# Performance work log

Hardware: AMD Instinct MI355X
Metric: run time of the kernel (lower is better)

## Reference

```python
import jax, jax.numpy as jnp
import numpy as np
from jax import lax

EPS = 1e-8
DN = ('NCHW', 'OIHW', 'NCHW')


def setup_inputs() -> dict:
    key = jax.random.key(0)
    k1, k2 = jax.random.split(key)
    inputs = jax.random.normal(k1, (16, 3, 512, 512), dtype=jnp.float32)
    template = jax.random.normal(k2, (16, 3, 21, 21), dtype=jnp.float32)
    return {"inputs": inputs, "template": template}


def _normalize_template(template):
    # Z-normalize each (batch, channel) plane independently, then divide by
    # patch element count (matches NCC.__init__).
    B, C, th, tw = template.shape
    t = template.reshape(B, C, th * tw)
    t = t - jnp.mean(t, axis=-1, keepdims=True)
    t = t / (jnp.std(t, axis=-1, keepdims=True) + EPS)  # ddof=0 == unbiased=False
    return t.reshape(B, C, th, tw) / (th * tw)


def reference(inputs, template):
    B, C, H, W = inputs.shape
    th, tw = template.shape[2], template.shape[3]
    nt = _normalize_template(template)

    # Per-(b,c) depthwise cross-correlation (the grouped conv with eye-masked
    # weights is exactly a depthwise conv with per-sample filters).
    x = inputs.reshape(1, B * C, H, W)
    w = nt.reshape(B * C, 1, th, tw)
    res = lax.conv_general_dilated(x, w, (1, 1), 'VALID',
                                   dimension_numbers=DN,
                                   feature_group_count=B * C)
    res = res.reshape(B, C, res.shape[2], res.shape[3])  # (B,C,Hout,Wout)

    # Local (patch) std per channel via box filter (shared across batch).
    box = jnp.full((C, 1, th, tw), 1.0 / (th * tw), dtype=inputs.dtype)
    mean = lax.conv_general_dilated(inputs, box, (1, 1), 'VALID',
                                    dimension_numbers=DN, feature_group_count=C)
    mean_sq = lax.conv_general_dilated(inputs * inputs, box, (1, 1), 'VALID',
                                       dimension_numbers=DN, feature_group_count=C)
    std = jnp.sqrt(mean_sq - mean * mean + EPS)

    return res / (std + EPS)
```

## Files before the change

### kernel.cpp

```cpp
#include <hip/hip_runtime.h>
#include <math.h>

typedef __attribute__((ext_vector_type(8)))  short short8;
typedef __attribute__((ext_vector_type(16))) float f32x16;

#define NPLANE 48
#define H 512
#define W 512
#define TH 21
#define OH 492
#define OW 492
#define EPSF 1e-8f

#define STRIDE 168
#define SEG_ROWS 84

#define BONES_HOFF (4128768u / 2)

__device__ inline unsigned short f2bf(float f) {
    unsigned u = __float_as_uint(f);
    return (unsigned short)((u + 0x7FFFu + ((u >> 16) & 1u)) >> 16);
}
__device__ inline float bf2f(unsigned s) {
    return __uint_as_float(s << 16);
}
__device__ inline unsigned cvtpk(float lo, float hi) {
    unsigned r;
    asm("v_cvt_pk_bf16_f32 %0, %1, %2" : "=v"(r) : "v"(lo), "v"(hi));
    return r;
}

__global__ void build_b_kernel(const float* __restrict__ tpl,
                               unsigned short* __restrict__ ws16) {
    __shared__ float sm[2];
    const int plane = blockIdx.x;
    const float* t = tpl + plane * 441;
    const int tid = threadIdx.x;
    if (tid < 64) {
        float s = 0.f, s2 = 0.f;
        for (int k = tid; k < 441; k += 64) {
            float x = t[k];
            s += x; s2 += x * x;
        }
#pragma unroll
        for (int o = 32; o >= 1; o >>= 1) {
            s  += __shfl_down(s, o);
            s2 += __shfl_down(s2, o);
        }
        if (tid == 0) {
            float mean = s / 441.f;
            float var = fmaxf(s2 / 441.f - mean * mean, 0.f);
            sm[0] = mean;
            sm[1] = 1.f / ((sqrtf(var) + EPSF) * 441.f);
        }
    }
    __syncthreads();
    const float mean = sm[0], scale = sm[1];

    unsigned short* bc = ws16 + (size_t)plane * 43008;
    for (int i = tid; i < 43008; i += 256) {
        int j = i & 7, lane = (i >> 3) & 63, s = (i >> 9) & 3, u = i >> 11;
        int k = ((lane >> 5) << 3) + j, n = lane & 31;
        int v = 16 * s + k - n;
        float val = (v >= 0 && v < TH) ? (t[u * 21 + v] - mean) * scale : 0.f;
        bc[i] = f2bf(val);
    }
    if (plane == 0) {
        unsigned short* bo = ws16 + BONES_HOFF;
        const unsigned short one = f2bf(1.f);
        for (int i = tid; i < 2048; i += 256) {
            int j = i & 7, lane = (i >> 3) & 63, s = (i >> 9) & 3;
            int k = ((lane >> 5) << 3) + j, n = lane & 31;
            int v = 16 * s + k - n;
            bo[i] = (v >= 0 && v < TH) ? one : (unsigned short)0;
        }
    }
}

__global__ __launch_bounds__(512, 6) void ncc_fused_kernel(
    const float* __restrict__ in, const unsigned short* __restrict__ ws16,
    float* __restrict__ out) {
    __shared__ short seg[SEG_ROWS * STRIDE];
    __shared__ short vbuf[64 * STRIDE];

    const int plane = blockIdx.z;
    const int x0 = blockIdx.x * 128;
    const int y0 = blockIdx.y * 64;
    const int tid = threadIdx.x;
    const int lane = tid & 63;
    const int wid = tid >> 6;
    const int tr = wid & 1;
    const int tc = wid >> 1;
    const float* src = in + (size_t)plane * H * W;

    for (int i = tid; i < SEG_ROWS * 20; i += 512) {
        int row = i / 20, s8 = i - row * 20;
        int gy = y0 + row, gx = x0 + s8 * 8;
        if (gy < H && gx + 7 < W) {
            float4 a = *(const float4*)(src + gy * W + gx);
            float4 b = *(const float4*)(src + gy * W + gx + 4);
            uint4 v;
            v.x = cvtpk(a.x, a.y);
            v.y = cvtpk(a.z, a.w);
            v.z = cvtpk(b.x, b.y);
            v.w = cvtpk(b.z, b.w);
            *(uint4*)&seg[row * STRIDE + s8 * 8] = v;
        } else {
            short8 val;
#pragma unroll
            for (int e = 0; e < 8; ++e) {
                float xv = (gy < H && gx + e < W) ? src[gy * W + gx + e] : 0.f;
                val[e] = (short)f2bf(xv);
            }
            *(short8*)&seg[row * STRIDE + s8 * 8] = val;
        }
    }
    __syncthreads();

    const int m = lane & 31;
    const int half = lane >> 5;
    const int abase = (tr * 32 + m) * STRIDE + tc * 32 + half * 8;
    const unsigned short* bc = ws16 + (size_t)plane * 43008 + lane * 8;

    f32x16 acc;
#pragma unroll
    for (int e = 0; e < 16; ++e) acc[e] = 0.f;

    auto corr_step = [&](int u, short8* bf) {
        short8 af[4];
#pragma unroll
        for (int s = 0; s < 4; ++s)
            af[s] = *(const short8*)&seg[abase + u * STRIDE + s * 16];
#pragma unroll
        for (int s = 0; s < 4; ++s)
            acc = __builtin_amdgcn_mfma_f32_32x32x16_bf16(af[s], bf[s], acc,
                                                          0, 0, 0);
    };

    short8 bA[4], bB[4];
#pragma unroll
    for (int s = 0; s < 4; ++s)
        bA[s] = *(const short8*)(bc + s * 512);

    for (int u = 0; u < TH - 1; u += 2) {
#pragma unroll
        for (int s = 0; s < 4; ++s)
            bB[s] = *(const short8*)(bc + ((u + 1) * 4 + s) * 512);
        corr_step(u, bA);
#pragma unroll
        for (int s = 0; s < 4; ++s)
            bA[s] = *(const short8*)(bc + ((u + 2) * 4 + s) * 512);
        corr_step(u + 1, bB);
    }
    corr_step(TH - 1, bA);

    const unsigned short* bo16 = ws16 + BONES_HOFF + lane * 8;
    short8 bones[4];
#pragma unroll
    for (int s = 0; s < 4; ++s)
        bones[s] = *(const short8*)(bo16 + s * 512);

    auto vpass = [&](bool sq) {
        if (tid < 320) {
            const int q = tid / 80;
            const int c2 = (tid - q * 80) * 2;
            const int base = q * 16;
            float s0 = 0.f, s1 = 0.f;
#pragma unroll
            for (int r = 0; r < 20; ++r) {
                unsigned p = *(const unsigned*)&seg[(base + r) * STRIDE + c2];
                float a = bf2f(p & 0xffffu), b = bf2f(p >> 16);
                if (sq) { s0 = fmaf(a, a, s0); s1 = fmaf(b, b, s1); }
                else    { s0 += a; s1 += b; }
            }
#pragma unroll
            for (int yb = 0; yb < 16; yb += 8) {
                unsigned pin[8], pout[8];
#pragma unroll
                for (int r = 0; r < 8; ++r) {
                    pin[r]  = *(const unsigned*)
                        &seg[(base + yb + r + 20) * STRIDE + c2];
                    pout[r] = *(const unsigned*)
                        &seg[(base + yb + r) * STRIDE + c2];
                }
#pragma unroll
                for (int r = 0; r < 8; ++r) {
                    float a = bf2f(pin[r] & 0xffffu), b = bf2f(pin[r] >> 16);
                    if (sq) { s0 = fmaf(a, a, s0); s1 = fmaf(b, b, s1); }
                    else    { s0 += a; s1 += b; }
                    *(unsigned*)&vbuf[(base + yb + r) * STRIDE + c2] =
                        cvtpk(s0, s1);
                    float c = bf2f(pout[r] & 0xffffu), d = bf2f(pout[r] >> 16);
                    if (sq) { s0 = fmaf(-c, c, s0); s1 = fmaf(-d, d, s1); }
                    else    { s0 -= c; s1 -= d; }
                }
            }
        }
    };

    vpass(false);
    __syncthreads();

    f32x16 aS;
#pragma unroll
    for (int e = 0; e < 16; ++e) aS[e] = 0.f;
#pragma unroll
    for (int s = 0; s < 4; ++s) {
        short8 vf = *(const short8*)&vbuf[abase + s * 16];
        aS = __builtin_amdgcn_mfma_f32_32x32x16_bf16(vf, bones[s], aS,
                                                     0, 0, 0);
    }
    __syncthreads();

    vpass(true);
    __syncthreads();

    f32x16 aQ;
#pragma unroll
    for (int e = 0; e < 16; ++e) aQ[e] = 0.f;
#pragma unroll
    for (int s = 0; s < 4; ++s) {
        short8 qf = *(const short8*)&vbuf[abase + s * 16];
        aQ = __builtin_amdgcn_mfma_f32_32x32x16_bf16(qf, bones[s], aQ,
                                                     0, 0, 0);
    }

    const float invn = 1.f / 441.f;
    float* outp = out + (size_t)plane * OH * OW;
    const int gx = x0 + tc * 32 + m;
    if (gx < OW) {
#pragma unroll
        for (int r = 0; r < 16; ++r) {
            int gy = y0 + tr * 32 + (r & 3) + ((r >> 2) << 3) + half * 4;
            if (gy < OH) {
                float mean = aS[r] * invn;
                float msq = aQ[r] * invn;
                float var = fmaf(-mean, mean, msq) + EPSF;
                outp[(size_t)gy * OW + gx] =
                    acc[r] * __builtin_amdgcn_rsqf(var);
            }
        }
    }
}

extern "C" void kernel_launch(void* const* d_in, const int* in_sizes, int n_in,
                              void* d_out, int out_size, void* d_ws,
                              size_t ws_size, hipStream_t stream) {
    const float* inputs = (const float*)d_in[0];
    const float* tmpl = (const float*)d_in[1];
    float* out = (float*)d_out;
    unsigned short* ws16 = (unsigned short*)d_ws;

    build_b_kernel<<<NPLANE, 256, 0, stream>>>(tmpl, ws16);
    ncc_fused_kernel<<<dim3(4, 8, NPLANE), 512, 0, stream>>>(inputs, ws16, out);
}
```

Baseline: 167.2 us.

## Process two row tiles per block with register prefetch of next input segment

Each block now handles two vertically stacked 64-row output tiles instead of one, which halves the grid. While the first tile is being correlated, the input rows for the second tile are loaded into registers, then converted to bf16 and written into shared memory after the first tile's compute finishes. The goal is to hide global load latency behind MFMA work and to amortise the bones/B-fragment setup. In exchange it uses more registers, lowers the occupancy target from 6 to 4 blocks, and leaves fewer blocks to spread across the CUs.

```diff
diff --git a/kernel.cpp b/kernel.cpp
--- a/kernel.cpp
+++ b/kernel.cpp
@@ -77,7 +77,7 @@
     }
 }
 
-__global__ __launch_bounds__(512, 6) void ncc_fused_kernel(
+__global__ __launch_bounds__(512, 4) void ncc_fused_kernel(
     const float* __restrict__ in, const unsigned short* __restrict__ ws16,
     float* __restrict__ out) {
     __shared__ short seg[SEG_ROWS * STRIDE];
@@ -85,7 +85,7 @@
 
     const int plane = blockIdx.z;
     const int x0 = blockIdx.x * 128;
-    const int y0 = blockIdx.y * 64;
+    const int yb = blockIdx.y * 128;
     const int tid = threadIdx.x;
     const int lane = tid & 63;
     const int wid = tid >> 6;
@@ -95,7 +95,7 @@
 
     for (int i = tid; i < SEG_ROWS * 20; i += 512) {
         int row = i / 20, s8 = i - row * 20;
-        int gy = y0 + row, gx = x0 + s8 * 8;
+        int gy = yb + row, gx = x0 + s8 * 8;
         if (gy < H && gx + 7 < W) {
             float4 a = *(const float4*)(src + gy * W + gx);
             float4 b = *(const float4*)(src + gy * W + gx + 4);
@@ -115,50 +115,19 @@
             *(short8*)&seg[row * STRIDE + s8 * 8] = val;
         }
     }
-    __syncthreads();
 
     const int m = lane & 31;
     const int half = lane >> 5;
     const int abase = (tr * 32 + m) * STRIDE + tc * 32 + half * 8;
     const unsigned short* bc = ws16 + (size_t)plane * 43008 + lane * 8;
 
-    f32x16 acc;
-#pragma unroll
-    for (int e = 0; e < 16; ++e) acc[e] = 0.f;
-
-    auto corr_step = [&](int u, short8* bf) {
-        short8 af[4];
-#pragma unroll
-        for (int s = 0; s < 4; ++s)
-            af[s] = *(const short8*)&seg[abase + u * STRIDE + s * 16];
-#pragma unroll
-        for (int s = 0; s < 4; ++s)
-            acc = __builtin_amdgcn_mfma_f32_32x32x16_bf16(af[s], bf[s], acc,
-                                                          0, 0, 0);
-    };
-
-    short8 bA[4], bB[4];
-#pragma unroll
-    for (int s = 0; s < 4; ++s)
-        bA[s] = *(const short8*)(bc + s * 512);
-
-    for (int u = 0; u < TH - 1; u += 2) {
-#pragma unroll
-        for (int s = 0; s < 4; ++s)
-            bB[s] = *(const short8*)(bc + ((u + 1) * 4 + s) * 512);
-        corr_step(u, bA);
-#pragma unroll
-        for (int s = 0; s < 4; ++s)
-            bA[s] = *(const short8*)(bc + ((u + 2) * 4 + s) * 512);
-        corr_step(u + 1, bB);
-    }
-    corr_step(TH - 1, bA);
-
     const unsigned short* bo16 = ws16 + BONES_HOFF + lane * 8;
     short8 bones[4];
 #pragma unroll
     for (int s = 0; s < 4; ++s)
         bones[s] = *(const short8*)(bo16 + s * 512);
+
+    __syncthreads();
 
     auto vpass = [&](bool sq) {
         if (tid < 320) {
@@ -174,21 +143,21 @@
                 else    { s0 += a; s1 += b; }
             }
 #pragma unroll
-            for (int yb = 0; yb < 16; yb += 8) {
+            for (int yy = 0; yy < 16; yy += 8) {
                 unsigned pin[8], pout[8];
 #pragma unroll
                 for (int r = 0; r < 8; ++r) {
                     pin[r]  = *(const unsigned*)
-                        &seg[(base + yb + r + 20) * STRIDE + c2];
+                        &seg[(base + yy + r + 20) * STRIDE + c2];
                     pout[r] = *(const unsigned*)
-                        &seg[(base + yb + r) * STRIDE + c2];
+                        &seg[(base + yy + r) * STRIDE + c2];
                 }
 #pragma unroll
                 for (int r = 0; r < 8; ++r) {
                     float a = bf2f(pin[r] & 0xffffu), b = bf2f(pin[r] >> 16);
                     if (sq) { s0 = fmaf(a, a, s0); s1 = fmaf(b, b, s1); }
                     else    { s0 += a; s1 += b; }
-                    *(unsigned*)&vbuf[(base + yb + r) * STRIDE + c2] =
+                    *(unsigned*)&vbuf[(base + yy + r) * STRIDE + c2] =
                         cvtpk(s0, s1);
                     float c = bf2f(pout[r] & 0xffffu), d = bf2f(pout[r] >> 16);
                     if (sq) { s0 = fmaf(-c, c, s0); s1 = fmaf(-d, d, s1); }
@@ -198,48 +167,131 @@
         }
     };
 
-    vpass(false);
-    __syncthreads();
-
-    f32x16 aS;
-#pragma unroll
-    for (int e = 0; e < 16; ++e) aS[e] = 0.f;
-#pragma unroll
-    for (int s = 0; s < 4; ++s) {
-        short8 vf = *(const short8*)&vbuf[abase + s * 16];
-        aS = __builtin_amdgcn_mfma_f32_32x32x16_bf16(vf, bones[s], aS,
-                                                     0, 0, 0);
-    }
-    __syncthreads();
-
-    vpass(true);
-    __syncthreads();
-
-    f32x16 aQ;
-#pragma unroll
-    for (int e = 0; e < 16; ++e) aQ[e] = 0.f;
-#pragma unroll
-    for (int s = 0; s < 4; ++s) {
-        short8 qf = *(const short8*)&vbuf[abase + s * 16];
-        aQ = __builtin_amdgcn_mfma_f32_32x32x16_bf16(qf, bones[s], aQ,
-                                                     0, 0, 0);
-    }
-
-    const float invn = 1.f / 441.f;
-    float* outp = out + (size_t)plane * OH * OW;
-    const int gx = x0 + tc * 32 + m;
-    if (gx < OW) {
+    for (int ty = 0; ty < 2; ++ty) {
+        const int y0 = yb + ty * 64;
+
+        float4 ldA[4], ldB[4];
+        if (ty == 0) {
+#pragma unroll
+            for (int k = 0; k < 4; ++k) {
+                ldA[k] = make_float4(0.f, 0.f, 0.f, 0.f);
+                ldB[k] = make_float4(0.f, 0.f, 0.f, 0.f);
+                int i = tid + k * 512;
+                if (i < SEG_ROWS * 20) {
+                    int row = i / 20, s8 = i - row * 20;
+                    int gy = yb + 64 + row, gx = x0 + s8 * 8;
+                    if (gy < H && gx + 7 < W) {
+                        ldA[k] = *(const float4*)(src + gy * W + gx);
+                        ldB[k] = *(const float4*)(src + gy * W + gx + 4);
+                    } else {
+                        float t[8];
+#pragma unroll
+                        for (int e = 0; e < 8; ++e)
+                            t[e] = (gy < H && gx + e < W)
+                                       ? src[gy * W + gx + e] : 0.f;
+                        ldA[k] = make_float4(t[0], t[1], t[2], t[3]);
+                        ldB[k] = make_float4(t[4], t[5], t[6], t[7]);
+                    }
+                }
+            }
+        }
+
+        f32x16 acc;
+#pragma unroll
+        for (int e = 0; e < 16; ++e) acc[e] = 0.f;
+
+        auto corr_step = [&](int u, short8* bf) {
+            short8 af[4];
+#pragma unroll
+            for (int s = 0; s < 4; ++s)
+                af[s] = *(const short8*)&seg[abase + u * STRIDE + s * 16];
+#pragma unroll
+            for (int s = 0; s < 4; ++s)
+                acc = __builtin_amdgcn_mfma_f32_32x32x16_bf16(af[s], bf[s],
+                                                              acc, 0, 0, 0);
+        };
+
+        short8 bA[4], bB[4];
+#pragma unroll
+        for (int s = 0; s < 4; ++s)
+            bA[s] = *(const short8*)(bc + s * 512);
+
+        for (int u = 0; u < TH - 1; u += 2) {
+#pragma unroll
+            for (int s = 0; s < 4; ++s)
+                bB[s] = *(const short8*)(bc + ((u + 1) * 4 + s) * 512);
+            corr_step(u, bA);
+#pragma unroll
+            for (int s = 0; s < 4; ++s)
+                bA[s] = *(const short8*)(bc + ((u + 2) * 4 + s) * 512);
+            corr_step(u + 1, bB);
+        }
+        corr_step(TH - 1, bA);
+
+        vpass(false);
+        __syncthreads();
+
+        f32x16 aS;
+#pragma unroll
+        for (int e = 0; e < 16; ++e) aS[e] = 0.f;
+#pragma unroll
+        for (int s = 0; s < 4; ++s) {
+            short8 vf = *(const short8*)&vbuf[abase + s * 16];
+            aS = __builtin_amdgcn_mfma_f32_32x32x16_bf16(vf, bones[s], aS,
+                                                         0, 0, 0);
+        }
+        __syncthreads();
+
+        vpass(true);
+        __syncthreads();
+
+        f32x16 aQ;
+#pragma unroll
+        for (int e = 0; e < 16; ++e) aQ[e] = 0.f;
+#pragma unroll
+        for (int s = 0; s < 4; ++s) {
+            short8 qf = *(const short8*)&vbuf[abase + s * 16];
+            aQ = __builtin_amdgcn_mfma_f32_32x32x16_bf16(qf, bones[s], aQ,
+                                                         0, 0, 0);
+        }
+
+        if (ty == 0) {
+#pragma unroll
+            for (int k = 0; k < 4; ++k) {
+                int i = tid + k * 512;
+                if (i < SEG_ROWS * 20) {
+                    int row = i / 20, s8 = i - row * 20;
+                    uint4 v;
+                    v.x = cvtpk(ldA[k].x, ldA[k].y);
+                    v.y = cvtpk(ldA[k].z, ldA[k].w);
+                    v.z = cvtpk(ldB[k].x, ldB[k].y);
+                    v.w = cvtpk(ldB[k].z, ldB[k].w);
+                    *(uint4*)&seg[row * STRIDE + s8 * 8] = v;
+                }
+            }
+        }
+
+        const float invn = 1.f / 441.f;
+        float* outp = out + (size_t)plane * OH * OW;
+        float vout[16];
 #pragma unroll
         for (int r = 0; r < 16; ++r) {
-            int gy = y0 + tr * 32 + (r & 3) + ((r >> 2) << 3) + half * 4;
-            if (gy < OH) {
-                float mean = aS[r] * invn;
-                float msq = aQ[r] * invn;
-                float var = fmaf(-mean, mean, msq) + EPSF;
-                outp[(size_t)gy * OW + gx] =
-                    acc[r] * __builtin_amdgcn_rsqf(var);
-            }
-        }
+            float mean = aS[r] * invn;
+            float msq = aQ[r] * invn;
+            float var = fmaf(-mean, mean, msq) + EPSF;
+            vout[r] = acc[r] * __builtin_amdgcn_rsqf(var);
+        }
+        const int gx = x0 + tc * 32 + m;
+        if (gx < OW) {
+#pragma unroll
+            for (int r = 0; r < 16; ++r) {
+                int gy = y0 + tr * 32 + (r & 3) + ((r >> 2) << 3) + half * 4;
+                if (gy < OH)
+                    outp[(size_t)gy * OW + gx] = vout[r];
+            }
+        }
+
+        __syncthreads();
     }
 }
 
@@ -252,5 +304,5 @@
     unsigned short* ws16 = (unsigned short*)d_ws;
 
     build_b_kernel<<<NPLANE, 256, 0, stream>>>(tmpl, ws16);
-    ncc_fused_kernel<<<dim3(4, 8, NPLANE), 512, 0, stream>>>(inputs, ws16, out);
-}
+    ncc_fused_kernel<<<dim3(4, 4, NPLANE), 512, 0, stream>>>(inputs, ws16, out);
+}
```

New measurement: 583.8 us. 3.49x slower.

## Compute box-sum and box-square passes concurrently across all waves with separate buffers

Applied to the files above, without the earlier changes.

The sum and sum-of-squares vertical box passes move into separate LDS buffers and are spread over all 8 waves, 640 work units in total. The serial sequence of two vpass phases with four barriers becomes one phase with a single barrier. The ones-matrix B-fragment load is hoisted before the first barrier, and the two reduction MFMAs are interleaved. LDS use per block grows by one 64x168 buffer, and launch bounds drop from 6 to 4 blocks per CU, which may lower occupancy.

```diff
diff --git a/kernel.cpp b/kernel.cpp
--- a/kernel.cpp
+++ b/kernel.cpp
@@ -77,11 +77,12 @@
     }
 }
 
-__global__ __launch_bounds__(512, 6) void ncc_fused_kernel(
+__global__ __launch_bounds__(512, 4) void ncc_fused_kernel(
     const float* __restrict__ in, const unsigned short* __restrict__ ws16,
     float* __restrict__ out) {
     __shared__ short seg[SEG_ROWS * STRIDE];
-    __shared__ short vbuf[64 * STRIDE];
+    __shared__ short vsum[64 * STRIDE];
+    __shared__ short vsq[64 * STRIDE];
 
     const int plane = blockIdx.z;
     const int x0 = blockIdx.x * 128;
@@ -115,13 +116,20 @@
             *(short8*)&seg[row * STRIDE + s8 * 8] = val;
         }
     }
-    __syncthreads();
 
     const int m = lane & 31;
     const int half = lane >> 5;
     const int abase = (tr * 32 + m) * STRIDE + tc * 32 + half * 8;
     const unsigned short* bc = ws16 + (size_t)plane * 43008 + lane * 8;
 
+    const unsigned short* bo16 = ws16 + BONES_HOFF + lane * 8;
+    short8 bones[4];
+#pragma unroll
+    for (int s = 0; s < 4; ++s)
+        bones[s] = *(const short8*)(bo16 + s * 512);
+
+    __syncthreads();
+
     f32x16 acc;
 #pragma unroll
     for (int e = 0; e < 16; ++e) acc[e] = 0.f;
@@ -154,91 +162,80 @@
     }
     corr_step(TH - 1, bA);
 
-    const unsigned short* bo16 = ws16 + BONES_HOFF + lane * 8;
-    short8 bones[4];
-#pragma unroll
-    for (int s = 0; s < 4; ++s)
-        bones[s] = *(const short8*)(bo16 + s * 512);
-
-    auto vpass = [&](bool sq) {
-        if (tid < 320) {
-            const int q = tid / 80;
-            const int c2 = (tid - q * 80) * 2;
-            const int base = q * 16;
-            float s0 = 0.f, s1 = 0.f;
-#pragma unroll
-            for (int r = 0; r < 20; ++r) {
-                unsigned p = *(const unsigned*)&seg[(base + r) * STRIDE + c2];
-                float a = bf2f(p & 0xffffu), b = bf2f(p >> 16);
-                if (sq) { s0 = fmaf(a, a, s0); s1 = fmaf(b, b, s1); }
-                else    { s0 += a; s1 += b; }
+    auto unit = [&](int U) {
+        const int p = U / 320;
+        const int rem = U - p * 320;
+        const int q = rem / 80;
+        const int c2 = (rem - q * 80) * 2;
+        const int base = q * 16;
+        short* dst = p ? vsq : vsum;
+        float s0 = 0.f, s1 = 0.f;
+#pragma unroll
+        for (int r = 0; r < 20; ++r) {
+            unsigned pk = *(const unsigned*)&seg[(base + r) * STRIDE + c2];
+            float a = bf2f(pk & 0xffffu), b = bf2f(pk >> 16);
+            if (p) { s0 = fmaf(a, a, s0); s1 = fmaf(b, b, s1); }
+            else   { s0 += a; s1 += b; }
+        }
+#pragma unroll
+        for (int yy = 0; yy < 16; yy += 8) {
+            unsigned pin[8], pout[8];
+#pragma unroll
+            for (int r = 0; r < 8; ++r) {
+                pin[r]  = *(const unsigned*)
+                    &seg[(base + yy + r + 20) * STRIDE + c2];
+                pout[r] = *(const unsigned*)
+                    &seg[(base + yy + r) * STRIDE + c2];
             }
 #pragma unroll
-            for (int yb = 0; yb < 16; yb += 8) {
-                unsigned pin[8], pout[8];
-#pragma unroll
-                for (int r = 0; r < 8; ++r) {
-                    pin[r]  = *(const unsigned*)
-                        &seg[(base + yb + r + 20) * STRIDE + c2];
-                    pout[r] = *(const unsigned*)
-                        &seg[(base + yb + r) * STRIDE + c2];
-                }
-#pragma unroll
-                for (int r = 0; r < 8; ++r) {
-                    float a = bf2f(pin[r] & 0xffffu), b = bf2f(pin[r] >> 16);
-                    if (sq) { s0 = fmaf(a, a, s0); s1 = fmaf(b, b, s1); }
-                    else    { s0 += a; s1 += b; }
-                    *(unsigned*)&vbuf[(base + yb + r) * STRIDE + c2] =
-                        cvtpk(s0, s1);
-                    float c = bf2f(pout[r] & 0xffffu), d = bf2f(pout[r] >> 16);
-                    if (sq) { s0 = fmaf(-c, c, s0); s1 = fmaf(-d, d, s1); }
-                    else    { s0 -= c; s1 -= d; }
-                }
+            for (int r = 0; r < 8; ++r) {
+                float a = bf2f(pin[r] & 0xffffu), b = bf2f(pin[r] >> 16);
+                if (p) { s0 = fmaf(a, a, s0); s1 = fmaf(b, b, s1); }
+                else   { s0 += a; s1 += b; }
+                *(unsigned*)&dst[(base + yy + r) * STRIDE + c2] =
+                    cvtpk(s0, s1);
+                float c = bf2f(pout[r] & 0xffffu), d = bf2f(pout[r] >> 16);
+                if (p) { s0 = fmaf(-c, c, s0); s1 = fmaf(-d, d, s1); }
+                else   { s0 -= c; s1 -= d; }
             }
         }
     };
 
-    vpass(false);
+    unit(wid * 80 + lane);
+    if (lane < 16) unit(wid * 80 + 64 + lane);
+
     __syncthreads();
 
-    f32x16 aS;
-#pragma unroll
-    for (int e = 0; e < 16; ++e) aS[e] = 0.f;
+    f32x16 aS, aQ;
+#pragma unroll
+    for (int e = 0; e < 16; ++e) { aS[e] = 0.f; aQ[e] = 0.f; }
 #pragma unroll
     for (int s = 0; s < 4; ++s) {
-        short8 vf = *(const short8*)&vbuf[abase + s * 16];
+        short8 vf = *(const short8*)&vsum[abase + s * 16];
+        short8 qf = *(const short8*)&vsq[abase + s * 16];
         aS = __builtin_amdgcn_mfma_f32_32x32x16_bf16(vf, bones[s], aS,
                                                      0, 0, 0);
-    }
-    __syncthreads();
-
-    vpass(true);
-    __syncthreads();
-
-    f32x16 aQ;
-#pragma unroll
-    for (int e = 0; e < 16; ++e) aQ[e] = 0.f;
-#pragma unroll
-    for (int s = 0; s < 4; ++s) {
-        short8 qf = *(const short8*)&vbuf[abase + s * 16];
         aQ = __builtin_amdgcn_mfma_f32_32x32x16_bf16(qf, bones[s], aQ,
                                                      0, 0, 0);
     }
 
     const float invn = 1.f / 441.f;
     float* outp = out + (size_t)plane * OH * OW;
+    float vout[16];
+#pragma unroll
+    for (int r = 0; r < 16; ++r) {
+        float mean = aS[r] * invn;
+        float msq = aQ[r] * invn;
+        float var = fmaf(-mean, mean, msq) + EPSF;
+        vout[r] = acc[r] * __builtin_amdgcn_rsqf(var);
+    }
     const int gx = x0 + tc * 32 + m;
     if (gx < OW) {
 #pragma unroll
         for (int r = 0; r < 16; ++r) {
             int gy = y0 + tr * 32 + (r & 3) + ((r >> 2) << 3) + half * 4;
-            if (gy < OH) {
-                float mean = aS[r] * invn;
-                float msq = aQ[r] * invn;
-                float var = fmaf(-mean, mean, msq) + EPSF;
-                outp[(size_t)gy * OW + gx] =
-                    acc[r] * __builtin_amdgcn_rsqf(var);
-            }
+            if (gy < OH)
+                outp[(size_t)gy * OW + gx] = vout[r];
         }
     }
 }
```

Measured after the change: 166.0 us. Within noise of the previous version (-0.7%).

## Overlap correlation MFMA with box-sum passes reading fp32 input from global

Applied to the files above, without the earlier changes.

Box-sum vertical passes now read fp32 input straight from global memory instead of the bf16 LDS tile. The correlation MFMA loop is placed before or after the vpass depending on a parity bit of the block's linear index. Co-resident blocks are meant to mix MFMA work with VALU/memory work, and the box statistics gain fp32 input precision. In exchange, each block re-reads about 84 input rows from global twice, and the later correlation in half of the blocks keeps the accumulator live across the vpasses, adding register pressure at launch bound 6.

```diff
diff --git a/kernel.cpp b/kernel.cpp
--- a/kernel.cpp
+++ b/kernel.cpp
@@ -92,6 +92,9 @@
     const int tr = wid & 1;
     const int tc = wid >> 1;
     const float* src = in + (size_t)plane * H * W;
+
+    const int linear = blockIdx.x + 4 * blockIdx.y + 32 * blockIdx.z;
+    const int par = (linear >> 8) & 1;
 
     for (int i = tid; i < SEG_ROWS * 20; i += 512) {
         int row = i / 20, s8 = i - row * 20;
@@ -115,82 +118,92 @@
             *(short8*)&seg[row * STRIDE + s8 * 8] = val;
         }
     }
-    __syncthreads();
 
     const int m = lane & 31;
     const int half = lane >> 5;
     const int abase = (tr * 32 + m) * STRIDE + tc * 32 + half * 8;
     const unsigned short* bc = ws16 + (size_t)plane * 43008 + lane * 8;
 
-    f32x16 acc;
-#pragma unroll
-    for (int e = 0; e < 16; ++e) acc[e] = 0.f;
-
-    auto corr_step = [&](int u, short8* bf) {
-        short8 af[4];
-#pragma unroll
-        for (int s = 0; s < 4; ++s)
-            af[s] = *(const short8*)&seg[abase + u * STRIDE + s * 16];
-#pragma unroll
-        for (int s = 0; s < 4; ++s)
-            acc = __builtin_amdgcn_mfma_f32_32x32x16_bf16(af[s], bf[s], acc,
-                                                          0, 0, 0);
-    };
-
-    short8 bA[4], bB[4];
-#pragma unroll
-    for (int s = 0; s < 4; ++s)
-        bA[s] = *(const short8*)(bc + s * 512);
-
-    for (int u = 0; u < TH - 1; u += 2) {
-#pragma unroll
-        for (int s = 0; s < 4; ++s)
-            bB[s] = *(const short8*)(bc + ((u + 1) * 4 + s) * 512);
-        corr_step(u, bA);
-#pragma unroll
-        for (int s = 0; s < 4; ++s)
-            bA[s] = *(const short8*)(bc + ((u + 2) * 4 + s) * 512);
-        corr_step(u + 1, bB);
-    }
-    corr_step(TH - 1, bA);
-
     const unsigned short* bo16 = ws16 + BONES_HOFF + lane * 8;
     short8 bones[4];
 #pragma unroll
     for (int s = 0; s < 4; ++s)
         bones[s] = *(const short8*)(bo16 + s * 512);
 
-    auto vpass = [&](bool sq) {
+    f32x16 acc;
+#pragma unroll
+    for (int e = 0; e < 16; ++e) acc[e] = 0.f;
+
+    auto corr_all = [&]() {
+        auto corr_step = [&](int u, short8* bf) {
+            short8 af[4];
+#pragma unroll
+            for (int s = 0; s < 4; ++s)
+                af[s] = *(const short8*)&seg[abase + u * STRIDE + s * 16];
+#pragma unroll
+            for (int s = 0; s < 4; ++s)
+                acc = __builtin_amdgcn_mfma_f32_32x32x16_bf16(af[s], bf[s],
+                                                              acc, 0, 0, 0);
+        };
+        short8 bA[4], bB[4];
+#pragma unroll
+        for (int s = 0; s < 4; ++s)
+            bA[s] = *(const short8*)(bc + s * 512);
+        for (int u = 0; u < TH - 1; u += 2) {
+#pragma unroll
+            for (int s = 0; s < 4; ++s)
+                bB[s] = *(const short8*)(bc + ((u + 1) * 4 + s) * 512);
+            corr_step(u, bA);
+#pragma unroll
+            for (int s = 0; s < 4; ++s)
+                bA[s] = *(const short8*)(bc + ((u + 2) * 4 + s) * 512);
+            corr_step(u + 1, bB);
+        }
+        corr_step(TH - 1, bA);
+    };
+
+    auto vpassG = [&](bool sq) {
         if (tid < 320) {
             const int q = tid / 80;
             const int c2 = (tid - q * 80) * 2;
             const int base = q * 16;
+            const int gx = x0 + c2;
+            const bool colok = (gx + 1) < W;
+            const float* col = src + gx;
             float s0 = 0.f, s1 = 0.f;
 #pragma unroll
             for (int r = 0; r < 20; ++r) {
-                unsigned p = *(const unsigned*)&seg[(base + r) * STRIDE + c2];
-                float a = bf2f(p & 0xffffu), b = bf2f(p >> 16);
+                int gy = y0 + base + r;
+                float a = 0.f, b = 0.f;
+                if (gy < H && colok) {
+                    float2 v = *(const float2*)(col + (size_t)gy * W);
+                    a = v.x; b = v.y;
+                }
                 if (sq) { s0 = fmaf(a, a, s0); s1 = fmaf(b, b, s1); }
                 else    { s0 += a; s1 += b; }
             }
 #pragma unroll
-            for (int yb = 0; yb < 16; yb += 8) {
-                unsigned pin[8], pout[8];
+            for (int yy = 0; yy < 16; yy += 8) {
+                float2 vin[8], vout[8];
 #pragma unroll
                 for (int r = 0; r < 8; ++r) {
-                    pin[r]  = *(const unsigned*)
-                        &seg[(base + yb + r + 20) * STRIDE + c2];
-                    pout[r] = *(const unsigned*)
-                        &seg[(base + yb + r) * STRIDE + c2];
+                    int gyi = y0 + base + yy + r + 20;
+                    int gyo = y0 + base + yy + r;
+                    vin[r] = make_float2(0.f, 0.f);
+                    vout[r] = make_float2(0.f, 0.f);
+                    if (gyi < H && colok)
+                        vin[r] = *(const float2*)(col + (size_t)gyi * W);
+                    if (gyo < H && colok)
+                        vout[r] = *(const float2*)(col + (size_t)gyo * W);
                 }
 #pragma unroll
                 for (int r = 0; r < 8; ++r) {
-                    float a = bf2f(pin[r] & 0xffffu), b = bf2f(pin[r] >> 16);
+                    float a = vin[r].x, b = vin[r].y;
                     if (sq) { s0 = fmaf(a, a, s0); s1 = fmaf(b, b, s1); }
                     else    { s0 += a; s1 += b; }
-                    *(unsigned*)&vbuf[(base + yb + r) * STRIDE + c2] =
+                    *(unsigned*)&vbuf[(base + yy + r) * STRIDE + c2] =
                         cvtpk(s0, s1);
-                    float c = bf2f(pout[r] & 0xffffu), d = bf2f(pout[r] >> 16);
+                    float c = vout[r].x, d = vout[r].y;
                     if (sq) { s0 = fmaf(-c, c, s0); s1 = fmaf(-d, d, s1); }
                     else    { s0 -= c; s1 -= d; }
                 }
@@ -198,21 +211,26 @@
         }
     };
 
-    vpass(false);
-    __syncthreads();
-
     f32x16 aS;
-#pragma unroll
-    for (int e = 0; e < 16; ++e) aS[e] = 0.f;
-#pragma unroll
-    for (int s = 0; s < 4; ++s) {
-        short8 vf = *(const short8*)&vbuf[abase + s * 16];
-        aS = __builtin_amdgcn_mfma_f32_32x32x16_bf16(vf, bones[s], aS,
-                                                     0, 0, 0);
-    }
-    __syncthreads();
-
-    vpass(true);
+    auto boxS = [&]() {
+#pragma unroll
+        for (int e = 0; e < 16; ++e) aS[e] = 0.f;
+#pragma unroll
+        for (int s = 0; s < 4; ++s) {
+            short8 vf = *(const short8*)&vbuf[abase + s * 16];
+            aS = __builtin_amdgcn_mfma_f32_32x32x16_bf16(vf, bones[s], aS,
+                                                         0, 0, 0);
+        }
+    };
+
+    __syncthreads();
+    if (!par) { corr_all(); vpassG(false); }
+    else      { vpassG(false); }
+    __syncthreads();
+    boxS();
+    __syncthreads();
+    if (!par) { vpassG(true); }
+    else      { vpassG(true); corr_all(); }
     __syncthreads();
 
     f32x16 aQ;
@@ -227,18 +245,21 @@
 
     const float invn = 1.f / 441.f;
     float* outp = out + (size_t)plane * OH * OW;
+    float vout[16];
+#pragma unroll
+    for (int r = 0; r < 16; ++r) {
+        float mean = aS[r] * invn;
+        float msq = aQ[r] * invn;
+        float var = fmaf(-mean, mean, msq) + EPSF;
+        vout[r] = acc[r] * __builtin_amdgcn_rsqf(var);
+    }
     const int gx = x0 + tc * 32 + m;
     if (gx < OW) {
 #pragma unroll
         for (int r = 0; r < 16; ++r) {
             int gy = y0 + tr * 32 + (r & 3) + ((r >> 2) << 3) + half * 4;
-            if (gy < OH) {
-                float mean = aS[r] * invn;
-                float msq = aQ[r] * invn;
-                float var = fmaf(-mean, mean, msq) + EPSF;
-                outp[(size_t)gy * OW + gx] =
-                    acc[r] * __builtin_amdgcn_rsqf(var);
-            }
+            if (gy < OH)
+                outp[(size_t)gy * OW + gx] = vout[r];
         }
     }
 }
```

Measured after the change: 289.3 us. 1.73x slower.
